# Kernel tuning notes

Hardware: AMD Instinct MI355X
Metric: run time of the kernel (lower is better)

## Reference

```python
import jax, jax.numpy as jnp
import numpy as np

DIM = 512
NUM_HEADS = 8
DIM_HEAD = 64
INNER = NUM_HEADS * DIM_HEAD  # 512
EPS = 1e-5


def setup_inputs() -> dict:
    key = jax.random.key(0)
    ks = jax.random.split(key, 6)
    B, H, W = 16, 64, 64
    x = jax.random.normal(ks[0], (B, DIM, H, W), dtype=jnp.float32)
    # 1x1 conv weights stored as [out, in]
    w_qkv = jax.random.normal(ks[1], (3 * INNER, DIM), dtype=jnp.float32) * (1.0 / np.sqrt(DIM))
    w_out = jax.random.normal(ks[2], (DIM, INNER), dtype=jnp.float32) * (1.0 / np.sqrt(INNER))
    b_out = jax.random.normal(ks[3], (DIM,), dtype=jnp.float32) * 0.01
    gamma = jnp.ones((DIM,), dtype=jnp.float32)
    beta = jnp.zeros((DIM,), dtype=jnp.float32)
    return {"x": x, "w_qkv": w_qkv, "w_out": w_out, "b_out": b_out,
            "gamma": gamma, "beta": beta}


def reference(x, w_qkv, w_out, b_out, gamma, beta):
    B, C, H, W = x.shape
    N = H * W
    # 1x1 conv == channel GEMM
    qkv = jnp.einsum('bchw,oc->bohw', x, w_qkv)            # [B, 3*INNER, H, W]
    qkv = qkv.reshape(B, 3, NUM_HEADS, DIM_HEAD, N)        # chunk along channel
    q, k, v = qkv[:, 0], qkv[:, 1], qkv[:, 2]              # each [B, h, Dh, N]
    # NOTE: faithful to source — attention over channel dim (Dh x Dh), not N x N
    scores = jnp.einsum('bhdn,bhen->bhde', q, k) / np.sqrt(DIM_HEAD)
    attn = jax.nn.softmax(scores, axis=-1)                 # [B, h, Dh, Dh]
    out = jnp.einsum('bhde,bhen->bhdn', attn, v)           # [B, h, Dh, N]
    out = out.reshape(B, INNER, H, W)
    out = jnp.einsum('bchw,oc->bohw', out, w_out) + b_out[None, :, None, None]
    # GroupNorm with 1 group == per-sample layernorm over (C,H,W) with channel affine
    mean = jnp.mean(out, axis=(1, 2, 3), keepdims=True)
    var = jnp.var(out, axis=(1, 2, 3), keepdims=True)
    out = (out - mean) * jax.lax.rsqrt(var + EPS)
    out = out * gamma[None, :, None, None] + beta[None, :, None, None]
    return out
```

## Files before the change

### kernel.cpp

```cpp
#include <hip/hip_runtime.h>

typedef __bf16 bf16;
typedef __bf16 bf16x8 __attribute__((ext_vector_type(8)));
typedef __bf16 bf16x4 __attribute__((ext_vector_type(4)));
typedef float  f32x4  __attribute__((ext_vector_type(4)));

#define BATCH   16
#define CDIM    512
#define NSPAT   4096
#define QKV_M   1536
#define INNER   512

__device__ __forceinline__ void gld16(const bf16* g, const bf16* l) {
  __builtin_amdgcn_global_load_lds(
      (const __attribute__((address_space(1))) void*)g,
      (__attribute__((address_space(3))) void*)l, 16, 0, 0);
}

__global__ __launch_bounds__(256) void cast_f32_bf16_kernel(
    const float* __restrict__ in, bf16* __restrict__ out, int n4) {
  int i = blockIdx.x * 256 + threadIdx.x;
  if (i >= n4) return;
  float4 v = ((const float4*)in)[i];
  bf16x4 o = { (bf16)v.x, (bf16)v.y, (bf16)v.z, (bf16)v.w };
  *(bf16x4*)(out + (size_t)i * 4) = o;
}

__global__ __launch_bounds__(256) void transpose_cast_kernel(
    const float* __restrict__ x, bf16* __restrict__ xt) {
  __shared__ __attribute__((aligned(16))) bf16 T[64][72];
  int b = blockIdx.z, c0 = blockIdx.y * 64, n0 = blockIdx.x * 64;
  int t = threadIdx.x;
  const float* xp = x + ((size_t)b * CDIM + c0) * NSPAT + n0;
#pragma unroll
  for (int i = 0; i < 4; ++i) {
    int v = t + i * 256;
    int c = v >> 4, nq = (v & 15) * 4;
    float4 rd = *(const float4*)(xp + (size_t)c * NSPAT + nq);
    T[nq + 0][c] = (bf16)rd.x; T[nq + 1][c] = (bf16)rd.y;
    T[nq + 2][c] = (bf16)rd.z; T[nq + 3][c] = (bf16)rd.w;
  }
  __syncthreads();
  bf16* op = xt + ((size_t)b * NSPAT + n0) * CDIM + c0;
#pragma unroll
  for (int i = 0; i < 2; ++i) {
    int v = t + i * 256;
    int n = v >> 3, cc = (v & 7) * 8;
    *(bf16x8*)(op + (size_t)n * CDIM + cc) = *(const bf16x8*)&T[n][cc];
  }
}

template <int OUTMODE>
__global__ __launch_bounds__(256) void gemm_tn_kernel(
    const bf16* __restrict__ A, const bf16* __restrict__ Bt,
    void* __restrict__ Cout, const float* __restrict__ bias,
    float* __restrict__ part, int M, int N, int K) {
  __shared__ __attribute__((aligned(16))) bf16 smem[8192];

  int b  = blockIdx.z;
  int m0 = blockIdx.y * 128, n0 = blockIdx.x * 128;
  const bf16* Ab = A + (size_t)m0 * K;
  const bf16* Bb = Bt + ((size_t)b * N + n0) * K;

  int tid = threadIdx.x, lane = tid & 63, wid = tid >> 6;
  int wm = wid >> 1, wn = wid & 1, lm = lane & 15, kqd = lane >> 4;
  int srow = lane >> 2, skb = lane & 3;

  f32x4 acc[4][4] = {};

  for (int k0 = 0; k0 < K; k0 += 32) {
#pragma unroll
    for (int i = 0; i < 2; ++i) {
      int gi = wid * 2 + i;
      gld16(Ab + (size_t)(gi * 16 + srow) * K + k0 + skb * 8, smem + gi * 512);
      gld16(Bb + (size_t)(gi * 16 + srow) * K + k0 + skb * 8, smem + 4096 + gi * 512);
    }
    __syncthreads();
    bf16x8 af[4], bfr[4];
#pragma unroll
    for (int im = 0; im < 4; ++im)
      af[im] = *(const bf16x8*)&smem[(wm * 64 + im * 16 + lm) * 32 + kqd * 8];
#pragma unroll
    for (int in = 0; in < 4; ++in)
      bfr[in] = *(const bf16x8*)&smem[4096 + (wn * 64 + in * 16 + lm) * 32 + kqd * 8];
#pragma unroll
    for (int im = 0; im < 4; ++im)
#pragma unroll
      for (int in = 0; in < 4; ++in)
        acc[im][in] = __builtin_amdgcn_mfma_f32_16x16x32_bf16(af[im], bfr[in], acc[im][in], 0, 0, 0);
    __syncthreads();
  }

  if (OUTMODE == 0) {
    bf16* C = (bf16*)Cout + (size_t)b * M * N;
    bf16* Ws = smem + wid * 2048;
#pragma unroll
    for (int half = 0; half < 2; ++half) {
#pragma unroll
      for (int im2 = 0; im2 < 2; ++im2) {
        int im = half * 2 + im2;
#pragma unroll
        for (int in = 0; in < 4; ++in)
#pragma unroll
          for (int r = 0; r < 4; ++r)
            Ws[(im2 * 16 + kqd * 4 + r) * 64 + in * 16 + lm] = (bf16)acc[im][in][r];
      }
#pragma unroll
      for (int j = 0; j < 4; ++j) {
        int u = lane + j * 64;
        int row = u >> 3, cu = (u & 7) * 8;
        *(bf16x8*)(C + (size_t)(m0 + wm * 64 + half * 32 + row) * N + n0 + wn * 64 + cu) =
            *(const bf16x8*)&Ws[row * 64 + cu];
      }
    }
  } else {
    float* C = (float*)Cout + (size_t)b * M * N;
    float s = 0.f, s2 = 0.f;
#pragma unroll
    for (int im = 0; im < 4; ++im)
#pragma unroll
      for (int in = 0; in < 4; ++in) {
        int row = m0 + wm * 64 + im * 16 + kqd * 4;
        int col = n0 + wn * 64 + in * 16 + lm;
#pragma unroll
        for (int r = 0; r < 4; ++r) {
          float v = acc[im][in][r] + bias[row + r];
          C[(size_t)(row + r) * N + col] = v;
          s += v; s2 += v * v;
        }
      }
#pragma unroll
    for (int off = 32; off > 0; off >>= 1) {
      s  += __shfl_down(s, off, 64);
      s2 += __shfl_down(s2, off, 64);
    }
    __shared__ float red[8];
    if (lane == 0) { red[wid] = s; red[wid + 4] = s2; }
    __syncthreads();
    if (tid == 0) {
      atomicAdd(&part[b * 2],     red[0] + red[1] + red[2] + red[3]);
      atomicAdd(&part[b * 2 + 1], red[4] + red[5] + red[6] + red[7]);
    }
  }
}

__global__ __launch_bounds__(256) void attn_scores_kernel(
    const bf16* __restrict__ qkv, float* __restrict__ sc_part) {
  __shared__ __attribute__((aligned(16))) bf16 qs[4096];
  int chunk = blockIdx.x, bh = blockIdx.y, b = bh >> 3, h = bh & 7;
  const bf16* q = qkv + ((size_t)b * QKV_M + h * 64) * NSPAT + chunk * 512;
  const bf16* k = q + (size_t)INNER * NSPAT;

  int tid = threadIdx.x, lane = tid & 63, wid = tid >> 6;
  int lm = lane & 15, kqd = lane >> 4, d0 = wid * 16;
  int srow = lane >> 2, skb = lane & 3;

  f32x4 acc[4] = {};
  for (int n0 = 0; n0 < 512; n0 += 32) {
    gld16(q + (size_t)(wid * 16 + srow) * NSPAT + n0 + skb * 8, qs + wid * 512);
    gld16(k + (size_t)(wid * 16 + srow) * NSPAT + n0 + skb * 8, qs + 2048 + wid * 512);
    __syncthreads();
    bf16x8 a = *(const bf16x8*)&qs[(d0 + lm) * 32 + kqd * 8];
#pragma unroll
    for (int eb = 0; eb < 4; ++eb) {
      bf16x8 bb = *(const bf16x8*)&qs[2048 + (eb * 16 + lm) * 32 + kqd * 8];
      acc[eb] = __builtin_amdgcn_mfma_f32_16x16x32_bf16(a, bb, acc[eb], 0, 0, 0);
    }
    __syncthreads();
  }
  float* outp = sc_part + ((size_t)bh * 8 + chunk) * 4096;
#pragma unroll
  for (int eb = 0; eb < 4; ++eb)
#pragma unroll
    for (int r = 0; r < 4; ++r)
      outp[(d0 + kqd * 4 + r) * 64 + eb * 16 + lm] = acc[eb][r];
}

__global__ __launch_bounds__(256) void attn_softmax_kernel(
    const float* __restrict__ sc_part, bf16* __restrict__ attn_w) {
  __shared__ float ssum[64][65];
  int bh = blockIdx.x, t = threadIdx.x;
  const float* p = sc_part + (size_t)bh * 8 * 4096;
  float v[16];
#pragma unroll
  for (int j = 0; j < 16; ++j) v[j] = p[t + j * 256];
  for (int c = 1; c < 8; ++c)
#pragma unroll
    for (int j = 0; j < 16; ++j) v[j] += p[c * 4096 + t + j * 256];
#pragma unroll
  for (int j = 0; j < 16; ++j) {
    int q = t + j * 256;
    ssum[q >> 6][q & 63] = v[j];
  }
  __syncthreads();
  if (t < 64) {
    float mx = -1e30f;
    for (int e = 0; e < 64; ++e) mx = fmaxf(mx, ssum[t][e]);
    float s = 0.f;
    for (int e = 0; e < 64; ++e) {
      float ex = __expf((ssum[t][e] - mx) * 0.125f);
      ssum[t][e] = ex; s += ex;
    }
    float inv = 1.0f / s;
    bf16* ow = attn_w + (size_t)bh * 4096 + t * 64;
    for (int e = 0; e < 64; ++e) ow[e] = (bf16)(ssum[t][e] * inv);
  }
}

__global__ __launch_bounds__(256) void attn_pv_kernel(
    const bf16* __restrict__ qkv, const bf16* __restrict__ attn_w,
    bf16* __restrict__ attn_t) {
  __shared__ __attribute__((aligned(16))) bf16 aw[64 * 72];
  __shared__ __attribute__((aligned(16))) bf16 Vs[128 * 72];
  int chunk = blockIdx.x, bh = blockIdx.y, b = bh >> 3, h = bh & 7;
  const bf16* vmat = qkv + ((size_t)b * QKV_M + 2 * INNER + h * 64) * NSPAT + chunk * 512;
  bf16* outt = attn_t + ((size_t)b * NSPAT + chunk * 512) * INNER + h * 64;

  int tid = threadIdx.x, lane = tid & 63, wid = tid >> 6;
  int lm = lane & 15, kqd = lane >> 4, d0 = wid * 16;

#pragma unroll
  for (int i = 0; i < 2; ++i) {
    int v = tid + i * 256;
    *(bf16x8*)&aw[(v >> 3) * 72 + (v & 7) * 8] = *(const bf16x8*)(attn_w + (size_t)bh * 4096 + v * 8);
  }
  __syncthreads();
  bf16x8 a0 = *(const bf16x8*)&aw[(d0 + lm) * 72 + kqd * 8];
  bf16x8 a1 = *(const bf16x8*)&aw[(d0 + lm) * 72 + 32 + kqd * 8];

  for (int nc = 0; nc < 512; nc += 128) {
    __syncthreads();
#pragma unroll
    for (int i = 0; i < 4; ++i) {
      int v = i * 256 + tid;
      int e = v & 63, nn = (v >> 6) * 8;
      bf16x8 d = *(const bf16x8*)(vmat + (size_t)e * NSPAT + nc + nn);
#pragma unroll
      for (int j = 0; j < 8; ++j) Vs[(nn + j) * 72 + e] = d[j];
    }
    __syncthreads();
    f32x4 o[8];
#pragma unroll
    for (int nt = 0; nt < 8; ++nt) {
      bf16x8 b0 = *(const bf16x8*)&Vs[(nt * 16 + lm) * 72 + kqd * 8];
      bf16x8 b1 = *(const bf16x8*)&Vs[(nt * 16 + lm) * 72 + 32 + kqd * 8];
      o[nt] = (f32x4){0.f, 0.f, 0.f, 0.f};
      o[nt] = __builtin_amdgcn_mfma_f32_16x16x32_bf16(a0, b0, o[nt], 0, 0, 0);
      o[nt] = __builtin_amdgcn_mfma_f32_16x16x32_bf16(a1, b1, o[nt], 0, 0, 0);
    }
    __syncthreads();
#pragma unroll
    for (int nt = 0; nt < 8; ++nt) {
      bf16x4 ov = { (bf16)o[nt][0], (bf16)o[nt][1], (bf16)o[nt][2], (bf16)o[nt][3] };
      *(bf16x4*)&Vs[(nt * 16 + lm) * 72 + d0 + kqd * 4] = ov;
    }
    __syncthreads();
#pragma unroll
    for (int i = 0; i < 4; ++i) {
      int v = i * 256 + tid;
      int n = v >> 3, dc = (v & 7) * 8;
      *(bf16x8*)(outt + (size_t)(nc + n) * INNER + dc) = *(const bf16x8*)&Vs[n * 72 + dc];
    }
  }
}

__global__ void ln_stats_kernel(const float* __restrict__ part, float2* __restrict__ stats) {
  int b = threadIdx.x;
  if (b < 16) {
    const float invn = 1.0f / 2097152.0f;
    float mean = part[b * 2] * invn;
    float var  = part[b * 2 + 1] * invn - mean * mean;
    stats[b] = make_float2(mean, rsqrtf(var + 1e-5f));
  }
}

__global__ __launch_bounds__(256) void ln_apply_kernel(
    float* __restrict__ out, const float2* __restrict__ stats,
    const float* __restrict__ gamma, const float* __restrict__ beta) {
  size_t i4 = (size_t)blockIdx.x * 256 + threadIdx.x;
  size_t e  = i4 * 4;
  int b = (int)(e >> 21);
  int c = (int)((e >> 12) & 511);
  float2 st = stats[b];
  float g  = gamma[c] * st.y;
  float bb = beta[c] - st.x * g;
  float4* p = (float4*)out;
  float4 v = p[i4];
  v.x = v.x * g + bb; v.y = v.y * g + bb; v.z = v.z * g + bb; v.w = v.w * g + bb;
  p[i4] = v;
}

extern "C" void kernel_launch(void* const* d_in, const int* in_sizes, int n_in,
                              void* d_out, int out_size, void* d_ws, size_t ws_size,
                              hipStream_t stream) {
  const float* x      = (const float*)d_in[0];
  const float* w_qkv  = (const float*)d_in[1];
  const float* w_out  = (const float*)d_in[2];
  const float* b_out  = (const float*)d_in[3];
  const float* gamma  = (const float*)d_in[4];
  const float* beta   = (const float*)d_in[5];
  float* out = (float*)d_out;

  char* ws = (char*)d_ws;
  bf16*   xt      = (bf16*)(ws);
  float*  sc_part = (float*)(ws);
  bf16*   attn_w  = (bf16*)(ws + 16777216);
  bf16*   wqkvb   = (bf16*)(ws + 67108864);
  bf16*   woutb   = (bf16*)(ws + 68681728);
  bf16*   qkvb    = (bf16*)(ws + 69206016);
  bf16*   attn_t  = (bf16*)(ws + 270532608);
  float*  part    = (float*)(ws + 337641472);
  float2* stats   = (float2*)(ws + 337641600);

  hipMemsetAsync(part, 0, 128, stream);

  transpose_cast_kernel<<<dim3(64, 8, BATCH), 256, 0, stream>>>(x, xt);
  cast_f32_bf16_kernel<<<768, 256, 0, stream>>>(w_qkv, wqkvb, 196608);
  cast_f32_bf16_kernel<<<256, 256, 0, stream>>>(w_out, woutb, 65536);

  gemm_tn_kernel<0><<<dim3(32, 12, BATCH), 256, 0, stream>>>(
      wqkvb, xt, (void*)qkvb, nullptr, nullptr, QKV_M, NSPAT, CDIM);

  attn_scores_kernel<<<dim3(8, 128), 256, 0, stream>>>(qkvb, sc_part);
  attn_softmax_kernel<<<128, 256, 0, stream>>>(sc_part, attn_w);
  attn_pv_kernel<<<dim3(8, 128), 256, 0, stream>>>(qkvb, attn_w, attn_t);

  gemm_tn_kernel<1><<<dim3(32, 4, BATCH), 256, 0, stream>>>(
      woutb, attn_t, (void*)out, b_out, part, INNER, NSPAT, CDIM);

  ln_stats_kernel<<<1, 16, 0, stream>>>(part, stats);
  ln_apply_kernel<<<32768, 256, 0, stream>>>(out, stats, gamma, beta);
}
```

Baseline: 574.0 us.

## Emit V transposed from QKV GEMM and simplify attention kernels to direct loads

The QKV GEMM now writes the V block as [n, channel] to a separate buffer and Q/K as before but via swapped MFMA operands for direct bf16x4 stores, dropping the LDS staging epilogue. The PV kernel reads transposed V and attention weights straight from global memory with no LDS transpose, and the scores kernel loads Q/K directly without LDS or barriers. The output GEMM also uses swapped operands to emit float4 stores. This removes LDS round trips and syncs, but relies on uncoalesced-ish direct global loads and strided transposed V writes.

```diff
diff --git a/kernel.cpp b/kernel.cpp
--- a/kernel.cpp
+++ b/kernel.cpp
@@ -54,7 +54,8 @@
 __global__ __launch_bounds__(256) void gemm_tn_kernel(
     const bf16* __restrict__ A, const bf16* __restrict__ Bt,
     void* __restrict__ Cout, const float* __restrict__ bias,
-    float* __restrict__ part, int M, int N, int K) {
+    float* __restrict__ part, bf16* __restrict__ vT,
+    int M, int N, int K) {
   __shared__ __attribute__((aligned(16))) bf16 smem[8192];
 
   int b  = blockIdx.z;
@@ -65,6 +66,7 @@
   int tid = threadIdx.x, lane = tid & 63, wid = tid >> 6;
   int wm = wid >> 1, wn = wid & 1, lm = lane & 15, kqd = lane >> 4;
   int srow = lane >> 2, skb = lane & 3;
+  const bool vmode = (OUTMODE == 0) && (m0 >= 1024);
 
   f32x4 acc[4][4] = {};
 
@@ -83,51 +85,64 @@
 #pragma unroll
     for (int in = 0; in < 4; ++in)
       bfr[in] = *(const bf16x8*)&smem[4096 + (wn * 64 + in * 16 + lm) * 32 + kqd * 8];
-#pragma unroll
-    for (int im = 0; im < 4; ++im)
+    if (vmode) {
+#pragma unroll
+      for (int im = 0; im < 4; ++im)
+#pragma unroll
+        for (int in = 0; in < 4; ++in)
+          acc[im][in] = __builtin_amdgcn_mfma_f32_16x16x32_bf16(af[im], bfr[in], acc[im][in], 0, 0, 0);
+    } else {
 #pragma unroll
       for (int in = 0; in < 4; ++in)
-        acc[im][in] = __builtin_amdgcn_mfma_f32_16x16x32_bf16(af[im], bfr[in], acc[im][in], 0, 0, 0);
+#pragma unroll
+        for (int im = 0; im < 4; ++im)
+          acc[in][im] = __builtin_amdgcn_mfma_f32_16x16x32_bf16(bfr[in], af[im], acc[in][im], 0, 0, 0);
+    }
     __syncthreads();
   }
 
   if (OUTMODE == 0) {
-    bf16* C = (bf16*)Cout + (size_t)b * M * N;
-    bf16* Ws = smem + wid * 2048;
-#pragma unroll
-    for (int half = 0; half < 2; ++half) {
-#pragma unroll
-      for (int im2 = 0; im2 < 2; ++im2) {
-        int im = half * 2 + im2;
-#pragma unroll
-        for (int in = 0; in < 4; ++in)
-#pragma unroll
-          for (int r = 0; r < 4; ++r)
-            Ws[(im2 * 16 + kqd * 4 + r) * 64 + in * 16 + lm] = (bf16)acc[im][in][r];
-      }
-#pragma unroll
-      for (int j = 0; j < 4; ++j) {
-        int u = lane + j * 64;
-        int row = u >> 3, cu = (u & 7) * 8;
-        *(bf16x8*)(C + (size_t)(m0 + wm * 64 + half * 32 + row) * N + n0 + wn * 64 + cu) =
-            *(const bf16x8*)&Ws[row * 64 + cu];
-      }
+    if (!vmode) {
+      bf16* C = (bf16*)Cout + (size_t)b * 1024 * N;
+#pragma unroll
+      for (int in = 0; in < 4; ++in)
+#pragma unroll
+        for (int im = 0; im < 4; ++im) {
+          int m  = m0 + wm * 64 + im * 16 + lm;
+          int nb = n0 + wn * 64 + in * 16 + kqd * 4;
+          bf16x4 o = { (bf16)acc[in][im][0], (bf16)acc[in][im][1],
+                       (bf16)acc[in][im][2], (bf16)acc[in][im][3] };
+          *(bf16x4*)(C + (size_t)m * N + nb) = o;
+        }
+    } else {
+      bf16* Vt = vT + (size_t)b * N * 512;
+#pragma unroll
+      for (int im = 0; im < 4; ++im)
+#pragma unroll
+        for (int in = 0; in < 4; ++in) {
+          int e = (m0 - 1024) + wm * 64 + im * 16 + kqd * 4;
+          int n = n0 + wn * 64 + in * 16 + lm;
+          bf16x4 o = { (bf16)acc[im][in][0], (bf16)acc[im][in][1],
+                       (bf16)acc[im][in][2], (bf16)acc[im][in][3] };
+          *(bf16x4*)(Vt + (size_t)n * 512 + e) = o;
+        }
     }
   } else {
     float* C = (float*)Cout + (size_t)b * M * N;
     float s = 0.f, s2 = 0.f;
 #pragma unroll
-    for (int im = 0; im < 4; ++im)
-#pragma unroll
-      for (int in = 0; in < 4; ++in) {
-        int row = m0 + wm * 64 + im * 16 + kqd * 4;
-        int col = n0 + wn * 64 + in * 16 + lm;
-#pragma unroll
-        for (int r = 0; r < 4; ++r) {
-          float v = acc[im][in][r] + bias[row + r];
-          C[(size_t)(row + r) * N + col] = v;
-          s += v; s2 += v * v;
-        }
+    for (int in = 0; in < 4; ++in)
+#pragma unroll
+      for (int im = 0; im < 4; ++im) {
+        int m  = m0 + wm * 64 + im * 16 + lm;
+        int nb = n0 + wn * 64 + in * 16 + kqd * 4;
+        float bv = bias[m];
+        float4 o;
+        o.x = acc[in][im][0] + bv; o.y = acc[in][im][1] + bv;
+        o.z = acc[in][im][2] + bv; o.w = acc[in][im][3] + bv;
+        *(float4*)(C + (size_t)m * N + nb) = o;
+        s += o.x + o.y + o.z + o.w;
+        s2 += o.x * o.x + o.y * o.y + o.z * o.z + o.w * o.w;
       }
 #pragma unroll
     for (int off = 32; off > 0; off >>= 1) {
@@ -146,27 +161,22 @@
 
 __global__ __launch_bounds__(256) void attn_scores_kernel(
     const bf16* __restrict__ qkv, float* __restrict__ sc_part) {
-  __shared__ __attribute__((aligned(16))) bf16 qs[4096];
   int chunk = blockIdx.x, bh = blockIdx.y, b = bh >> 3, h = bh & 7;
-  const bf16* q = qkv + ((size_t)b * QKV_M + h * 64) * NSPAT + chunk * 512;
-  const bf16* k = q + (size_t)INNER * NSPAT;
+  const bf16* q = qkv + ((size_t)b * 1024 + h * 64) * NSPAT + chunk * 512;
+  const bf16* k = q + (size_t)512 * NSPAT;
 
   int tid = threadIdx.x, lane = tid & 63, wid = tid >> 6;
   int lm = lane & 15, kqd = lane >> 4, d0 = wid * 16;
-  int srow = lane >> 2, skb = lane & 3;
 
   f32x4 acc[4] = {};
+#pragma unroll 2
   for (int n0 = 0; n0 < 512; n0 += 32) {
-    gld16(q + (size_t)(wid * 16 + srow) * NSPAT + n0 + skb * 8, qs + wid * 512);
-    gld16(k + (size_t)(wid * 16 + srow) * NSPAT + n0 + skb * 8, qs + 2048 + wid * 512);
-    __syncthreads();
-    bf16x8 a = *(const bf16x8*)&qs[(d0 + lm) * 32 + kqd * 8];
+    bf16x8 a = *(const bf16x8*)(q + (size_t)(d0 + lm) * NSPAT + n0 + kqd * 8);
 #pragma unroll
     for (int eb = 0; eb < 4; ++eb) {
-      bf16x8 bb = *(const bf16x8*)&qs[2048 + (eb * 16 + lm) * 32 + kqd * 8];
+      bf16x8 bb = *(const bf16x8*)(k + (size_t)(eb * 16 + lm) * NSPAT + n0 + kqd * 8);
       acc[eb] = __builtin_amdgcn_mfma_f32_16x16x32_bf16(a, bb, acc[eb], 0, 0, 0);
     }
-    __syncthreads();
   }
   float* outp = sc_part + ((size_t)bh * 8 + chunk) * 4096;
 #pragma unroll
@@ -208,58 +218,41 @@
 }
 
 __global__ __launch_bounds__(256) void attn_pv_kernel(
-    const bf16* __restrict__ qkv, const bf16* __restrict__ attn_w,
+    const bf16* __restrict__ vT, const bf16* __restrict__ attn_w,
     bf16* __restrict__ attn_t) {
-  __shared__ __attribute__((aligned(16))) bf16 aw[64 * 72];
-  __shared__ __attribute__((aligned(16))) bf16 Vs[128 * 72];
-  int chunk = blockIdx.x, bh = blockIdx.y, b = bh >> 3, h = bh & 7;
-  const bf16* vmat = qkv + ((size_t)b * QKV_M + 2 * INNER + h * 64) * NSPAT + chunk * 512;
-  bf16* outt = attn_t + ((size_t)b * NSPAT + chunk * 512) * INNER + h * 64;
-
+  int bh = blockIdx.y, b = bh >> 3, h = bh & 7;
   int tid = threadIdx.x, lane = tid & 63, wid = tid >> 6;
-  int lm = lane & 15, kqd = lane >> 4, d0 = wid * 16;
-
-#pragma unroll
-  for (int i = 0; i < 2; ++i) {
-    int v = tid + i * 256;
-    *(bf16x8*)&aw[(v >> 3) * 72 + (v & 7) * 8] = *(const bf16x8*)(attn_w + (size_t)bh * 4096 + v * 8);
-  }
-  __syncthreads();
-  bf16x8 a0 = *(const bf16x8*)&aw[(d0 + lm) * 72 + kqd * 8];
-  bf16x8 a1 = *(const bf16x8*)&aw[(d0 + lm) * 72 + 32 + kqd * 8];
-
-  for (int nc = 0; nc < 512; nc += 128) {
-    __syncthreads();
-#pragma unroll
-    for (int i = 0; i < 4; ++i) {
-      int v = i * 256 + tid;
-      int e = v & 63, nn = (v >> 6) * 8;
-      bf16x8 d = *(const bf16x8*)(vmat + (size_t)e * NSPAT + nc + nn);
-#pragma unroll
-      for (int j = 0; j < 8; ++j) Vs[(nn + j) * 72 + e] = d[j];
-    }
-    __syncthreads();
-    f32x4 o[8];
-#pragma unroll
-    for (int nt = 0; nt < 8; ++nt) {
-      bf16x8 b0 = *(const bf16x8*)&Vs[(nt * 16 + lm) * 72 + kqd * 8];
-      bf16x8 b1 = *(const bf16x8*)&Vs[(nt * 16 + lm) * 72 + 32 + kqd * 8];
-      o[nt] = (f32x4){0.f, 0.f, 0.f, 0.f};
-      o[nt] = __builtin_amdgcn_mfma_f32_16x16x32_bf16(a0, b0, o[nt], 0, 0, 0);
-      o[nt] = __builtin_amdgcn_mfma_f32_16x16x32_bf16(a1, b1, o[nt], 0, 0, 0);
-    }
-    __syncthreads();
-#pragma unroll
-    for (int nt = 0; nt < 8; ++nt) {
-      bf16x4 ov = { (bf16)o[nt][0], (bf16)o[nt][1], (bf16)o[nt][2], (bf16)o[nt][3] };
-      *(bf16x4*)&Vs[(nt * 16 + lm) * 72 + d0 + kqd * 4] = ov;
-    }
-    __syncthreads();
-#pragma unroll
-    for (int i = 0; i < 4; ++i) {
-      int v = i * 256 + tid;
-      int n = v >> 3, dc = (v & 7) * 8;
-      *(bf16x8*)(outt + (size_t)(nc + n) * INNER + dc) = *(const bf16x8*)&Vs[n * 72 + dc];
+  int lm = lane & 15, kqd = lane >> 4;
+  int nbase = blockIdx.x * 256 + wid * 64;
+
+  const bf16* aw = attn_w + (size_t)bh * 4096;
+  const bf16* vp = vT + ((size_t)b * NSPAT) * 512 + h * 64;
+  bf16* op = attn_t + ((size_t)b * NSPAT) * 512 + h * 64;
+
+  bf16x8 af[4][2];
+#pragma unroll
+  for (int im = 0; im < 4; ++im)
+#pragma unroll
+    for (int hf = 0; hf < 2; ++hf)
+      af[im][hf] = *(const bf16x8*)(aw + (im * 16 + lm) * 64 + hf * 32 + kqd * 8);
+
+#pragma unroll
+  for (int nt = 0; nt < 4; ++nt) {
+    int n = nbase + nt * 16 + lm;
+    bf16x8 b0 = *(const bf16x8*)(vp + (size_t)n * 512 + kqd * 8);
+    bf16x8 b1 = *(const bf16x8*)(vp + (size_t)n * 512 + 32 + kqd * 8);
+    f32x4 o[4] = {};
+#pragma unroll
+    for (int im = 0; im < 4; ++im) {
+      o[im] = __builtin_amdgcn_mfma_f32_16x16x32_bf16(af[im][0], b0, o[im], 0, 0, 0);
+      o[im] = __builtin_amdgcn_mfma_f32_16x16x32_bf16(af[im][1], b1, o[im], 0, 0, 0);
+    }
+#pragma unroll
+    for (int im = 0; im < 4; ++im) {
+      int nn = nbase + nt * 16 + lm;
+      int d  = im * 16 + kqd * 4;
+      bf16x4 ov = { (bf16)o[im][0], (bf16)o[im][1], (bf16)o[im][2], (bf16)o[im][3] };
+      *(bf16x4*)(op + (size_t)nn * 512 + d) = ov;
     }
   }
 }
@@ -308,6 +301,7 @@
   bf16*   wqkvb   = (bf16*)(ws + 67108864);
   bf16*   woutb   = (bf16*)(ws + 68681728);
   bf16*   qkvb    = (bf16*)(ws + 69206016);
+  bf16*   vTb     = (bf16*)(ws + 203423744);
   bf16*   attn_t  = (bf16*)(ws + 270532608);
   float*  part    = (float*)(ws + 337641472);
   float2* stats   = (float2*)(ws + 337641600);
@@ -319,14 +313,14 @@
   cast_f32_bf16_kernel<<<256, 256, 0, stream>>>(w_out, woutb, 65536);
 
   gemm_tn_kernel<0><<<dim3(32, 12, BATCH), 256, 0, stream>>>(
-      wqkvb, xt, (void*)qkvb, nullptr, nullptr, QKV_M, NSPAT, CDIM);
+      wqkvb, xt, (void*)qkvb, nullptr, nullptr, vTb, QKV_M, NSPAT, CDIM);
 
   attn_scores_kernel<<<dim3(8, 128), 256, 0, stream>>>(qkvb, sc_part);
   attn_softmax_kernel<<<128, 256, 0, stream>>>(sc_part, attn_w);
-  attn_pv_kernel<<<dim3(8, 128), 256, 0, stream>>>(qkvb, attn_w, attn_t);
+  attn_pv_kernel<<<dim3(16, 128), 256, 0, stream>>>(vTb, attn_w, attn_t);
 
   gemm_tn_kernel<1><<<dim3(32, 4, BATCH), 256, 0, stream>>>(
-      woutb, attn_t, (void*)out, b_out, part, INNER, NSPAT, CDIM);
+      woutb, attn_t, (void*)out, b_out, part, nullptr, INNER, NSPAT, CDIM);
 
   ln_stats_kernel<<<1, 16, 0, stream>>>(part, stats);
   ln_apply_kernel<<<32768, 256, 0, stream>>>(out, stats, gamma, beta);
```

After: 668.9 us. 1.17x slower.

## Transpose GEMM MFMA operands for vectorized epilogue stores; drop LDS in attention scores

Applied to the files above, without the earlier changes.

The GEMM swaps the MFMA operand order so each lane holds four consecutive N-columns. The bf16 epilogue can then write 8-byte vectors into a padded LDS tile with stride 72, which avoids bank conflicts, and the f32 epilogue can issue float4 stores with a single bias load per fragment. The attention-scores kernel stops staging through shared memory and reads q/k fragments straight from global memory, which removes the block barriers but relies on L1/L2 to serve the redundant k loads across waves. The padding grows shared memory slightly, and the explicit waitcnt asm stands in for barriers within each wave's private LDS region.

```diff
diff --git a/kernel.cpp b/kernel.cpp
--- a/kernel.cpp
+++ b/kernel.cpp
@@ -55,7 +55,7 @@
     const bf16* __restrict__ A, const bf16* __restrict__ Bt,
     void* __restrict__ Cout, const float* __restrict__ bias,
     float* __restrict__ part, int M, int N, int K) {
-  __shared__ __attribute__((aligned(16))) bf16 smem[8192];
+  __shared__ __attribute__((aligned(16))) bf16 smem[9216];
 
   int b  = blockIdx.z;
   int m0 = blockIdx.y * 128, n0 = blockIdx.x * 128;
@@ -84,50 +84,55 @@
     for (int in = 0; in < 4; ++in)
       bfr[in] = *(const bf16x8*)&smem[4096 + (wn * 64 + in * 16 + lm) * 32 + kqd * 8];
 #pragma unroll
-    for (int im = 0; im < 4; ++im)
-#pragma unroll
-      for (int in = 0; in < 4; ++in)
-        acc[im][in] = __builtin_amdgcn_mfma_f32_16x16x32_bf16(af[im], bfr[in], acc[im][in], 0, 0, 0);
+    for (int in = 0; in < 4; ++in)
+#pragma unroll
+      for (int im = 0; im < 4; ++im)
+        acc[in][im] = __builtin_amdgcn_mfma_f32_16x16x32_bf16(bfr[in], af[im], acc[in][im], 0, 0, 0);
     __syncthreads();
   }
 
   if (OUTMODE == 0) {
     bf16* C = (bf16*)Cout + (size_t)b * M * N;
-    bf16* Ws = smem + wid * 2048;
+    bf16* Ws = smem + wid * 2304;
 #pragma unroll
     for (int half = 0; half < 2; ++half) {
 #pragma unroll
-      for (int im2 = 0; im2 < 2; ++im2) {
-        int im = half * 2 + im2;
-#pragma unroll
-        for (int in = 0; in < 4; ++in)
-#pragma unroll
-          for (int r = 0; r < 4; ++r)
-            Ws[(im2 * 16 + kqd * 4 + r) * 64 + in * 16 + lm] = (bf16)acc[im][in][r];
+      for (int imh = 0; imh < 2; ++imh) {
+        int im = half * 2 + imh;
+        int mloc = imh * 16 + lm;
+#pragma unroll
+        for (int in = 0; in < 4; ++in) {
+          bf16x4 o = { (bf16)acc[in][im][0], (bf16)acc[in][im][1],
+                       (bf16)acc[in][im][2], (bf16)acc[in][im][3] };
+          *(bf16x4*)&Ws[mloc * 72 + in * 16 + kqd * 4] = o;
+        }
       }
+      asm volatile("s_waitcnt lgkmcnt(0)");
 #pragma unroll
       for (int j = 0; j < 4; ++j) {
-        int u = lane + j * 64;
+        int u = j * 64 + lane;
         int row = u >> 3, cu = (u & 7) * 8;
         *(bf16x8*)(C + (size_t)(m0 + wm * 64 + half * 32 + row) * N + n0 + wn * 64 + cu) =
-            *(const bf16x8*)&Ws[row * 64 + cu];
+            *(const bf16x8*)&Ws[row * 72 + cu];
       }
+      asm volatile("s_waitcnt lgkmcnt(0)");
     }
   } else {
     float* C = (float*)Cout + (size_t)b * M * N;
     float s = 0.f, s2 = 0.f;
 #pragma unroll
-    for (int im = 0; im < 4; ++im)
-#pragma unroll
-      for (int in = 0; in < 4; ++in) {
-        int row = m0 + wm * 64 + im * 16 + kqd * 4;
-        int col = n0 + wn * 64 + in * 16 + lm;
-#pragma unroll
-        for (int r = 0; r < 4; ++r) {
-          float v = acc[im][in][r] + bias[row + r];
-          C[(size_t)(row + r) * N + col] = v;
-          s += v; s2 += v * v;
-        }
+    for (int in = 0; in < 4; ++in)
+#pragma unroll
+      for (int im = 0; im < 4; ++im) {
+        int m  = m0 + wm * 64 + im * 16 + lm;
+        int nb = n0 + wn * 64 + in * 16 + kqd * 4;
+        float bv = bias[m];
+        float4 o;
+        o.x = acc[in][im][0] + bv; o.y = acc[in][im][1] + bv;
+        o.z = acc[in][im][2] + bv; o.w = acc[in][im][3] + bv;
+        *(float4*)(C + (size_t)m * N + nb) = o;
+        s  += o.x + o.y + o.z + o.w;
+        s2 += o.x * o.x + o.y * o.y + o.z * o.z + o.w * o.w;
       }
 #pragma unroll
     for (int off = 32; off > 0; off >>= 1) {
@@ -146,27 +151,22 @@
 
 __global__ __launch_bounds__(256) void attn_scores_kernel(
     const bf16* __restrict__ qkv, float* __restrict__ sc_part) {
-  __shared__ __attribute__((aligned(16))) bf16 qs[4096];
   int chunk = blockIdx.x, bh = blockIdx.y, b = bh >> 3, h = bh & 7;
   const bf16* q = qkv + ((size_t)b * QKV_M + h * 64) * NSPAT + chunk * 512;
   const bf16* k = q + (size_t)INNER * NSPAT;
 
   int tid = threadIdx.x, lane = tid & 63, wid = tid >> 6;
   int lm = lane & 15, kqd = lane >> 4, d0 = wid * 16;
-  int srow = lane >> 2, skb = lane & 3;
 
   f32x4 acc[4] = {};
+#pragma unroll 2
   for (int n0 = 0; n0 < 512; n0 += 32) {
-    gld16(q + (size_t)(wid * 16 + srow) * NSPAT + n0 + skb * 8, qs + wid * 512);
-    gld16(k + (size_t)(wid * 16 + srow) * NSPAT + n0 + skb * 8, qs + 2048 + wid * 512);
-    __syncthreads();
-    bf16x8 a = *(const bf16x8*)&qs[(d0 + lm) * 32 + kqd * 8];
+    bf16x8 a = *(const bf16x8*)(q + (size_t)(d0 + lm) * NSPAT + n0 + kqd * 8);
 #pragma unroll
     for (int eb = 0; eb < 4; ++eb) {
-      bf16x8 bb = *(const bf16x8*)&qs[2048 + (eb * 16 + lm) * 32 + kqd * 8];
+      bf16x8 bb = *(const bf16x8*)(k + (size_t)(eb * 16 + lm) * NSPAT + n0 + kqd * 8);
       acc[eb] = __builtin_amdgcn_mfma_f32_16x16x32_bf16(a, bb, acc[eb], 0, 0, 0);
     }
-    __syncthreads();
   }
   float* outp = sc_part + ((size_t)bh * 8 + chunk) * 4096;
 #pragma unroll
```

New measurement: 586.5 us. 2.2% more time.
